# Performance work log

Hardware: AMD Instinct MI355X
Metric: run time of the kernel (lower is better)

The kernel has to match this reference:

```python
import jax, jax.numpy as jnp
import numpy as np

N_NODES = 100000
N_EDGES = 1600000
D = 128
N_LAYERS = 3  # GIN num_layers = n_layers + 1 with n_layers = 2
BN_EPS = 1e-5


def _batchnorm(x, gamma, beta):
    # Training-mode BatchNorm1d over the node axis (biased variance, as torch uses
    # for normalization).
    mean = jnp.mean(x, axis=0)
    var = jnp.mean((x - mean) ** 2, axis=0)
    return (x - mean) * jax.lax.rsqrt(var + BN_EPS) * gamma + beta


def setup_inputs() -> dict:
    key = jax.random.key(0)
    ks = jax.random.split(key, 5)
    features = jax.random.normal(ks[0], (N_NODES, D), dtype=jnp.float32)
    W = jax.random.normal(ks[1], (N_LAYERS, D, D), dtype=jnp.float32) * 0.05
    b = jnp.zeros((N_LAYERS, D), dtype=jnp.float32)
    eps = jnp.zeros((N_LAYERS,), dtype=jnp.float32)  # learn_eps init 0
    bn1_gamma = jnp.ones((N_LAYERS, D), dtype=jnp.float32)
    bn1_beta = jnp.zeros((N_LAYERS, D), dtype=jnp.float32)
    bn2_gamma = jnp.ones((N_LAYERS, D), dtype=jnp.float32)
    bn2_beta = jnp.zeros((N_LAYERS, D), dtype=jnp.float32)
    src = jax.random.randint(ks[2], (N_EDGES,), 0, N_NODES, dtype=jnp.int64 if jax.config.jax_enable_x64 else jnp.int32)
    dst = jax.random.randint(ks[3], (N_EDGES,), 0, N_NODES, dtype=jnp.int64 if jax.config.jax_enable_x64 else jnp.int32)
    return {
        'features': features, 'W': W, 'b': b, 'eps': eps,
        'bn1_gamma': bn1_gamma, 'bn1_beta': bn1_beta,
        'bn2_gamma': bn2_gamma, 'bn2_beta': bn2_beta,
        'src': src, 'dst': dst,
    }


def reference(features, W, b, eps, bn1_gamma, bn1_beta, bn2_gamma, bn2_beta, src, dst):
    n = features.shape[0]
    h = features
    hidden_rep = [h]
    for i in range(N_LAYERS):
        # GINConv, 'sum' aggregation: (1+eps)*h_v + sum_{u->v} h_u
        agg = jax.ops.segment_sum(h[src], dst, num_segments=n)
        z = (1.0 + eps[i]) * h + agg
        # ApplyNodeFunc: Linear (num_mlp_layers=1) -> BN -> ReLU
        z = z @ W[i] + b[i]
        z = jax.nn.relu(_batchnorm(z, bn1_gamma[i], bn1_beta[i]))
        # GIN.forward: outer BN -> ReLU
        z = jax.nn.relu(_batchnorm(z, bn2_gamma[i], bn2_beta[i]))
        h = z
        hidden_rep.append(h)
    # torch.stack(hidden_rep) -> [n_layers+2, N, D]
    return jnp.stack(hidden_rep, axis=0)
```

## Files before the change

### kernel.cpp

```cpp
#include <hip/hip_runtime.h>
#include <hip/hip_bf16.h>

#define DD 128

typedef __attribute__((ext_vector_type(8))) short bfrag8;
typedef __attribute__((ext_vector_type(4))) float f32x4;

__device__ __forceinline__ float bf16lo(unsigned int u) {
    union { unsigned int i; float f; } c; c.i = u << 16; return c.f;
}
__device__ __forceinline__ float bf16hi(unsigned int u) {
    union { unsigned int i; float f; } c; c.i = u & 0xffff0000u; return c.f;
}
__device__ __forceinline__ float bf16f(unsigned short u) {
    union { unsigned int i; float f; } c; c.i = ((unsigned int)u) << 16; return c.f;
}
__device__ __forceinline__ unsigned short f2bf(float f) {
    union { float f; unsigned int i; } c; c.f = f;
    unsigned int x = c.i;
    unsigned int r = (x + 0x7fffu + ((x >> 16) & 1u)) >> 16;
    return (unsigned short)r;
}

__global__ void k_setup(const int* __restrict__ dst, int* __restrict__ deg, int E,
                        const float* __restrict__ features, float* __restrict__ out0,
                        unsigned int* __restrict__ hb, int total4,
                        const float* __restrict__ W, unsigned short* __restrict__ Wt) {
    int gtid = blockIdx.x * blockDim.x + threadIdx.x;
    int gsz = gridDim.x * blockDim.x;
    for (int i = gtid; i < E; i += gsz) atomicAdd(&deg[dst[i]], 1);
    for (int i = gtid; i < total4; i += gsz) {
        float4 v = ((const float4*)features)[i];
        ((float4*)out0)[i] = v;
        unsigned int lo = (unsigned int)f2bf(v.x) | ((unsigned int)f2bf(v.y) << 16);
        unsigned int hi = (unsigned int)f2bf(v.z) | ((unsigned int)f2bf(v.w) << 16);
        ((uint2*)hb)[i] = make_uint2(lo, hi);
    }
    for (int i = gtid; i < 3 * 128 * 128; i += gsz) {
        int l = i >> 14, r = i & 16383, k = r >> 7, n = r & 127;
        Wt[(l << 14) + n * 128 + k] = f2bf(W[i]);
    }
}

__global__ void k_scan1(const int* __restrict__ deg, int* __restrict__ partials, int Nn) {
    __shared__ int sm[256];
    int tid = threadIdx.x;
    int base = (blockIdx.x << 10) + 4 * tid;
    int s = 0;
    if (base + 3 < Nn) {
        int4 v = *(const int4*)&deg[base];
        s = v.x + v.y + v.z + v.w;
    } else {
        for (int j = 0; j < 4; j++) if (base + j < Nn) s += deg[base + j];
    }
    sm[tid] = s;
    __syncthreads();
    for (int off = 128; off > 0; off >>= 1) {
        if (tid < off) sm[tid] += sm[tid + off];
        __syncthreads();
    }
    if (tid == 0) partials[blockIdx.x] = sm[0];
}

__global__ void k_scan3(const int* __restrict__ deg, const int* __restrict__ partials,
                        int* __restrict__ row_start, int Nn, int E, int nchunk) {
    __shared__ int sp[256];
    __shared__ int sm[256];
    int tid = threadIdx.x, c = blockIdx.x;
    int p = (tid < nchunk) ? partials[tid] : 0;
    sp[tid] = p;
    __syncthreads();
    for (int off = 1; off < 256; off <<= 1) {
        int t = (tid >= off) ? sp[tid - off] : 0;
        __syncthreads();
        sp[tid] += t;
        __syncthreads();
    }
    int chunkpref = (c == 0) ? 0 : sp[c - 1];

    int base = (c << 10) + 4 * tid;
    int d0 = 0, d1 = 0, d2 = 0, d3 = 0;
    if (base + 3 < Nn) {
        int4 v = *(const int4*)&deg[base];
        d0 = v.x; d1 = v.y; d2 = v.z; d3 = v.w;
    } else {
        if (base + 0 < Nn) d0 = deg[base + 0];
        if (base + 1 < Nn) d1 = deg[base + 1];
        if (base + 2 < Nn) d2 = deg[base + 2];
        if (base + 3 < Nn) d3 = deg[base + 3];
    }
    int ts = d0 + d1 + d2 + d3;
    sm[tid] = ts;
    __syncthreads();
    for (int off = 1; off < 256; off <<= 1) {
        int t = (tid >= off) ? sm[tid - off] : 0;
        __syncthreads();
        sm[tid] += t;
        __syncthreads();
    }
    int run = chunkpref + sm[tid] - ts;
    if (base + 0 < Nn) row_start[base + 0] = run; run += d0;
    if (base + 1 < Nn) row_start[base + 1] = run; run += d1;
    if (base + 2 < Nn) row_start[base + 2] = run; run += d2;
    if (base + 3 < Nn) row_start[base + 3] = run;
    if (c == 0 && tid == 0) row_start[Nn] = E;
}

__global__ void k_scatter(const int* __restrict__ src, const int* __restrict__ dst,
                          const int* __restrict__ row_start, int* __restrict__ cursor,
                          int* __restrict__ csr, int E) {
    int i = blockIdx.x * blockDim.x + threadIdx.x;
    if (i < E) {
        int d = dst[i];
        int pos = row_start[d] + atomicAdd(&cursor[d], 1);
        csr[pos] = src[i];
    }
}

__device__ __forceinline__ void acc_u4(float* acc, uint4 a) {
    acc[0] += bf16lo(a.x); acc[1] += bf16hi(a.x);
    acc[2] += bf16lo(a.y); acc[3] += bf16hi(a.y);
    acc[4] += bf16lo(a.z); acc[5] += bf16hi(a.z);
    acc[6] += bf16lo(a.w); acc[7] += bf16hi(a.w);
}

__global__ void k_gather(const unsigned int* __restrict__ hb, const int* __restrict__ row_start,
                         const int* __restrict__ csr, const float* __restrict__ eps, int layer,
                         unsigned int* __restrict__ zb, int Nn) {
    int wv = threadIdx.x >> 6, lane = threadIdx.x & 63;
    int v = blockIdx.x * 4 + wv;
    if (v >= Nn) return;
    int q = lane & 15;
    int slot = lane >> 4;
    const uint4* hb4 = (const uint4*)hb;
    float acc[8];
    #pragma unroll
    for (int j = 0; j < 8; j++) acc[j] = 0.f;

    int beg = row_start[v], end = row_start[v + 1];
    int e = beg;
    for (; e + 15 < end; e += 16) {
        int u0 = csr[e + slot];
        int u1 = csr[e + 4 + slot];
        int u2 = csr[e + 8 + slot];
        int u3 = csr[e + 12 + slot];
        uint4 a = hb4[(size_t)u0 * 16 + q];
        uint4 b = hb4[(size_t)u1 * 16 + q];
        uint4 c = hb4[(size_t)u2 * 16 + q];
        uint4 d = hb4[(size_t)u3 * 16 + q];
        acc_u4(acc, a); acc_u4(acc, b); acc_u4(acc, c); acc_u4(acc, d);
    }
    for (; e + 3 < end; e += 4) {
        int u = csr[e + slot];
        uint4 a = hb4[(size_t)u * 16 + q];
        acc_u4(acc, a);
    }
    {
        int r = end - e;
        if (slot < r) {
            int u = csr[e + slot];
            uint4 a = hb4[(size_t)u * 16 + q];
            acc_u4(acc, a);
        }
    }
    #pragma unroll
    for (int j = 0; j < 8; j++) {
        acc[j] += __shfl_xor(acc[j], 16);
        acc[j] += __shfl_xor(acc[j], 32);
    }
    if (slot == 0) {
        float e1 = 1.0f + eps[layer];
        uint4 hs = hb4[(size_t)v * 16 + q];
        float f0 = acc[0] + e1 * bf16lo(hs.x);
        float f1 = acc[1] + e1 * bf16hi(hs.x);
        float f2 = acc[2] + e1 * bf16lo(hs.y);
        float f3 = acc[3] + e1 * bf16hi(hs.y);
        float f4 = acc[4] + e1 * bf16lo(hs.z);
        float f5 = acc[5] + e1 * bf16hi(hs.z);
        float f6 = acc[6] + e1 * bf16lo(hs.w);
        float f7 = acc[7] + e1 * bf16hi(hs.w);
        uint4 o;
        o.x = (unsigned int)f2bf(f0) | ((unsigned int)f2bf(f1) << 16);
        o.y = (unsigned int)f2bf(f2) | ((unsigned int)f2bf(f3) << 16);
        o.z = (unsigned int)f2bf(f4) | ((unsigned int)f2bf(f5) << 16);
        o.w = (unsigned int)f2bf(f6) | ((unsigned int)f2bf(f7) << 16);
        ((uint4*)zb)[(size_t)v * 16 + q] = o;
    }
}

__launch_bounds__(256)
__global__ void k_gemm(const unsigned short* __restrict__ zb, const unsigned short* __restrict__ Wt,
                       const float* __restrict__ bias, int layer, unsigned short* __restrict__ yb,
                       float* __restrict__ stl, int Nn) {
    __shared__ unsigned short Al[64 * 136];
    int tid = threadIdx.x;
    int m0 = blockIdx.x * 64;
    #pragma unroll
    for (int p = 0; p < 4; p++) {
        int slot = p * 256 + tid;
        int r = slot >> 4, c = slot & 15;
        int grow = m0 + r;
        uint4 val = make_uint4(0, 0, 0, 0);
        if (grow < Nn) val = *(const uint4*)&zb[(size_t)grow * 128 + c * 8];
        *(uint4*)&Al[r * 136 + c * 8] = val;
    }
    __syncthreads();

    int lane = tid & 63, wv = tid >> 6;
    int tcol = lane & 15, quad = lane >> 4;
    const unsigned short* Wl = Wt + (layer << 14);
    f32x4 acc[4][2];
    #pragma unroll
    for (int a = 0; a < 4; a++)
        #pragma unroll
        for (int b2 = 0; b2 < 2; b2++) acc[a][b2] = (f32x4){0.f, 0.f, 0.f, 0.f};

    #pragma unroll
    for (int kk = 0; kk < 128; kk += 32) {
        int kb = kk + quad * 8;
        bfrag8 af[4], bf[2];
        #pragma unroll
        for (int mt = 0; mt < 4; mt++)
            af[mt] = *(const bfrag8*)&Al[(16 * mt + tcol) * 136 + kb];
        #pragma unroll
        for (int nt = 0; nt < 2; nt++)
            bf[nt] = *(const bfrag8*)&Wl[(32 * wv + 16 * nt + tcol) * 128 + kb];
        #pragma unroll
        for (int mt = 0; mt < 4; mt++)
            #pragma unroll
            for (int nt = 0; nt < 2; nt++)
                acc[mt][nt] = __builtin_amdgcn_mfma_f32_16x16x32_bf16(af[mt], bf[nt], acc[mt][nt], 0, 0, 0);
    }

    #pragma unroll
    for (int nt = 0; nt < 2; nt++) {
        int col = 32 * wv + 16 * nt + tcol;
        float bcol = bias[layer * 128 + col];
        float psum = 0.f, psq = 0.f;
        #pragma unroll
        for (int mt = 0; mt < 4; mt++) {
            #pragma unroll
            for (int r = 0; r < 4; r++) {
                int row = m0 + 16 * mt + quad * 4 + r;
                if (row < Nn) {
                    unsigned short u = f2bf(acc[mt][nt][r] + bcol);
                    yb[(size_t)row * 128 + col] = u;
                    float vr = bf16f(u);
                    psum += vr;
                    psq += vr * vr;
                }
            }
        }
        psum += __shfl_xor(psum, 16); psq += __shfl_xor(psq, 16);
        psum += __shfl_xor(psum, 32); psq += __shfl_xor(psq, 32);
        if (lane < 16) {
            atomicAdd(&stl[col], psum);
            atomicAdd(&stl[128 + col], psq);
        }
    }
}

__launch_bounds__(256)
__global__ void k_stats2(const unsigned short* __restrict__ yb, float* __restrict__ stl,
                         const float* __restrict__ g1, const float* __restrict__ b1,
                         int layer, int totalU8, float invN) {
    __shared__ float red[512];
    int tid = threadIdx.x;
    if (tid < 128) {
        float m = stl[tid] * invN;
        float var = stl[128 + tid] * invN - m * m;
        float rstd = rsqrtf(var + 1e-5f);
        float s = g1[layer * 128 + tid] * rstd;
        red[tid] = s;
        red[128 + tid] = b1[layer * 128 + tid] - m * s;
        red[256 + tid] = 0.f;
        red[384 + tid] = 0.f;
    }
    __syncthreads();
    int lane = tid & 63;
    int cbase = (8 * tid) & 127;
    float s1r[8], sh1r[8];
    #pragma unroll
    for (int j = 0; j < 8; j++) { s1r[j] = red[cbase + j]; sh1r[j] = red[128 + cbase + j]; }
    float ps[8], pq[8];
    #pragma unroll
    for (int j = 0; j < 8; j++) { ps[j] = 0.f; pq[j] = 0.f; }
    int gtid = blockIdx.x * 256 + tid;
    int gsz = gridDim.x * 256;
    const uint4* yb4 = (const uint4*)yb;
    for (int i = gtid; i < totalU8; i += gsz) {
        uint4 v = yb4[i];
        float f[8];
        f[0] = bf16lo(v.x); f[1] = bf16hi(v.x);
        f[2] = bf16lo(v.y); f[3] = bf16hi(v.y);
        f[4] = bf16lo(v.z); f[5] = bf16hi(v.z);
        f[6] = bf16lo(v.w); f[7] = bf16hi(v.w);
        #pragma unroll
        for (int j = 0; j < 8; j++) {
            float t = fmaxf(f[j] * s1r[j] + sh1r[j], 0.f);
            ps[j] += t; pq[j] += t * t;
        }
    }
    #pragma unroll
    for (int j = 0; j < 8; j++) {
        ps[j] += __shfl_xor(ps[j], 16);
        pq[j] += __shfl_xor(pq[j], 16);
        ps[j] += __shfl_xor(ps[j], 32);
        pq[j] += __shfl_xor(pq[j], 32);
    }
    if (lane < 16) {
        #pragma unroll
        for (int j = 0; j < 8; j++) {
            atomicAdd(&red[256 + cbase + j], ps[j]);
            atomicAdd(&red[384 + cbase + j], pq[j]);
        }
    }
    __syncthreads();
    if (tid < 128) {
        atomicAdd(&stl[256 + tid], red[256 + tid]);
        atomicAdd(&stl[384 + tid], red[384 + tid]);
    }
}

__launch_bounds__(256)
__global__ void k_apply(const unsigned short* __restrict__ yb, const float* __restrict__ stl,
                        const float* __restrict__ g1, const float* __restrict__ b1,
                        const float* __restrict__ g2, const float* __restrict__ b2,
                        int layer, float* __restrict__ outl, unsigned int* __restrict__ hb,
                        int totalU8, float invN) {
    __shared__ float red[512];
    int tid = threadIdx.x;
    if (tid < 128) {
        float m1 = stl[tid] * invN;
        float v1 = stl[128 + tid] * invN - m1 * m1;
        float r1 = rsqrtf(v1 + 1e-5f);
        float s1 = g1[layer * 128 + tid] * r1;
        red[tid] = s1;
        red[128 + tid] = b1[layer * 128 + tid] - m1 * s1;
        float m2 = stl[256 + tid] * invN;
        float v2 = stl[384 + tid] * invN - m2 * m2;
        float r2 = rsqrtf(v2 + 1e-5f);
        float s2 = g2[layer * 128 + tid] * r2;
        red[256 + tid] = s2;
        red[384 + tid] = b2[layer * 128 + tid] - m2 * s2;
    }
    __syncthreads();
    int cbase = (8 * tid) & 127;
    float s1a[8], sh1a[8], s2a[8], sh2a[8];
    #pragma unroll
    for (int j = 0; j < 8; j++) {
        s1a[j]  = red[cbase + j];       sh1a[j] = red[128 + cbase + j];
        s2a[j]  = red[256 + cbase + j]; sh2a[j] = red[384 + cbase + j];
    }
    int gtid = blockIdx.x * 256 + tid;
    int gsz = gridDim.x * 256;
    const uint4* yb4 = (const uint4*)yb;
    for (int i = gtid; i < totalU8; i += gsz) {
        uint4 v = yb4[i];
        float f[8];
        f[0] = bf16lo(v.x); f[1] = bf16hi(v.x);
        f[2] = bf16lo(v.y); f[3] = bf16hi(v.y);
        f[4] = bf16lo(v.z); f[5] = bf16hi(v.z);
        f[6] = bf16lo(v.w); f[7] = bf16hi(v.w);
        float o[8];
        #pragma unroll
        for (int j = 0; j < 8; j++) {
            float t = fmaxf(f[j] * s1a[j] + sh1a[j], 0.f);
            o[j] = fmaxf(t * s2a[j] + sh2a[j], 0.f);
        }
        ((float4*)outl)[2 * i]     = make_float4(o[0], o[1], o[2], o[3]);
        ((float4*)outl)[2 * i + 1] = make_float4(o[4], o[5], o[6], o[7]);
        uint4 hbv;
        hbv.x = (unsigned int)f2bf(o[0]) | ((unsigned int)f2bf(o[1]) << 16);
        hbv.y = (unsigned int)f2bf(o[2]) | ((unsigned int)f2bf(o[3]) << 16);
        hbv.z = (unsigned int)f2bf(o[4]) | ((unsigned int)f2bf(o[5]) << 16);
        hbv.w = (unsigned int)f2bf(o[6]) | ((unsigned int)f2bf(o[7]) << 16);
        ((uint4*)hb)[i] = hbv;
    }
}

extern "C" void kernel_launch(void* const* d_in, const int* in_sizes, int n_in,
                              void* d_out, int out_size, void* d_ws, size_t ws_size,
                              hipStream_t stream) {
    const float* features = (const float*)d_in[0];
    const float* W        = (const float*)d_in[1];
    const float* bias     = (const float*)d_in[2];
    const float* eps      = (const float*)d_in[3];
    const float* g1       = (const float*)d_in[4];
    const float* b1       = (const float*)d_in[5];
    const float* g2       = (const float*)d_in[6];
    const float* b2       = (const float*)d_in[7];
    const int*   src      = (const int*)d_in[8];
    const int*   dst      = (const int*)d_in[9];

    const int Nn = in_sizes[0] / DD;
    const int E  = in_sizes[8];
    float* out = (float*)d_out;

    char* w = (char*)d_ws;
    auto alloc = [&](size_t bytes) -> char* {
        char* p = w;
        w += (bytes + 255) & ~(size_t)255;
        return p;
    };
    int*   deg    = (int*)alloc((size_t)Nn * 4);
    int*   cursor = (int*)alloc((size_t)Nn * 4);
    float* stats  = (float*)alloc(3 * 512 * 4);
    char*  zero_end = w;
    int* row_start = (int*)alloc((size_t)(Nn + 1) * 4);
    int* partials  = (int*)alloc(1024);
    int* csr       = (int*)alloc((size_t)E * 4);
    unsigned int* hb = (unsigned int*)alloc((size_t)Nn * 64 * 4);
    unsigned int* zb = (unsigned int*)alloc((size_t)Nn * 64 * 4);
    unsigned short* Wt = (unsigned short*)alloc((size_t)3 * 128 * 128 * 2);
    unsigned short* yb = (unsigned short*)alloc((size_t)Nn * 128 * 2);

    const int total4 = Nn * DD / 4;
    const int totalU8 = Nn * DD / 8;
    const float invN = 1.0f / (float)Nn;
    const int nchunk = (Nn + 1023) / 1024;

    hipMemsetAsync(deg, 0, (size_t)(zero_end - (char*)deg), stream);

    k_setup<<<(E + 255) / 256, 256, 0, stream>>>(dst, deg, E, features, out, hb, total4, W, Wt);
    k_scan1<<<nchunk, 256, 0, stream>>>(deg, partials, Nn);
    k_scan3<<<nchunk, 256, 0, stream>>>(deg, partials, row_start, Nn, E, nchunk);
    k_scatter<<<(E + 255) / 256, 256, 0, stream>>>(src, dst, row_start, cursor, csr, E);

    for (int l = 0; l < 3; l++) {
        float* stl = stats + l * 512;
        float* outl = out + (size_t)(l + 1) * Nn * DD;
        k_gather<<<(Nn + 3) / 4, 256, 0, stream>>>(hb, row_start, csr, eps, l, zb, Nn);
        k_gemm<<<(Nn + 63) / 64, 256, 0, stream>>>((const unsigned short*)zb, Wt, bias, l, yb,
                                                   stl, Nn);
        k_stats2<<<512, 256, 0, stream>>>(yb, stl, g1, b1, l, totalU8, invN);
        k_apply<<<1024, 256, 0, stream>>>(yb, stl, g1, b1, g2, b2, l, outl, hb, totalU8, invN);
    }
}
```

Baseline: 833.8 us.

## Fuse GEMM, BN stats and apply into one persistent kernel with grid barriers

Replaces the separate GEMM, second-BN-stats and apply kernels with one kernel per layer. Each block computes two 64-row tiles, keeps the bf16 results in registers, and uses two software grid barriers to wait for the global BN statistics before applying the normalisations. This removes the yb round trip through global memory and two launches. The risks are a deadlock if all ~782 blocks cannot be co-resident (launch bounds 256,4 over 256 CUs), and that the final stores are now scalar and less coalesced.

```diff
diff --git a/kernel.cpp b/kernel.cpp
--- a/kernel.cpp
+++ b/kernel.cpp
@@ -188,13 +188,13 @@
     }
 }
 
-__launch_bounds__(256)
-__global__ void k_gemm(const unsigned short* __restrict__ zb, const unsigned short* __restrict__ Wt,
-                       const float* __restrict__ bias, int layer, unsigned short* __restrict__ yb,
-                       float* __restrict__ stl, int Nn) {
-    __shared__ unsigned short Al[64 * 136];
-    int tid = threadIdx.x;
-    int m0 = blockIdx.x * 64;
+__device__ __forceinline__ void layer_tile(const unsigned short* __restrict__ zb,
+                                           const unsigned short* __restrict__ Wl,
+                                           const float* __restrict__ bias, int layer,
+                                           float* __restrict__ stl, unsigned short* Al,
+                                           int m0, int Nn, int tid, int lane, int wv,
+                                           int tcol, int quad, unsigned int (&ypk)[4][2][2]) {
+    __syncthreads();
     #pragma unroll
     for (int p = 0; p < 4; p++) {
         int slot = p * 256 + tid;
@@ -206,9 +206,6 @@
     }
     __syncthreads();
 
-    int lane = tid & 63, wv = tid >> 6;
-    int tcol = lane & 15, quad = lane >> 4;
-    const unsigned short* Wl = Wt + (layer << 14);
     f32x4 acc[4][2];
     #pragma unroll
     for (int a = 0; a < 4; a++)
@@ -239,17 +236,18 @@
         float psum = 0.f, psq = 0.f;
         #pragma unroll
         for (int mt = 0; mt < 4; mt++) {
-            #pragma unroll
-            for (int r = 0; r < 4; r++) {
-                int row = m0 + 16 * mt + quad * 4 + r;
-                if (row < Nn) {
-                    unsigned short u = f2bf(acc[mt][nt][r] + bcol);
-                    yb[(size_t)row * 128 + col] = u;
-                    float vr = bf16f(u);
-                    psum += vr;
-                    psq += vr * vr;
-                }
-            }
+            unsigned short u0 = f2bf(acc[mt][nt][0] + bcol);
+            unsigned short u1 = f2bf(acc[mt][nt][1] + bcol);
+            unsigned short u2 = f2bf(acc[mt][nt][2] + bcol);
+            unsigned short u3 = f2bf(acc[mt][nt][3] + bcol);
+            ypk[mt][nt][0] = (unsigned int)u0 | ((unsigned int)u1 << 16);
+            ypk[mt][nt][1] = (unsigned int)u2 | ((unsigned int)u3 << 16);
+            int rowb = m0 + 16 * mt + quad * 4;
+            float v0 = bf16f(u0), v1 = bf16f(u1), v2 = bf16f(u2), v3 = bf16f(u3);
+            if (rowb + 0 < Nn) { psum += v0; psq += v0 * v0; }
+            if (rowb + 1 < Nn) { psum += v1; psq += v1 * v1; }
+            if (rowb + 2 < Nn) { psum += v2; psq += v2 * v2; }
+            if (rowb + 3 < Nn) { psum += v3; psq += v3 * v3; }
         }
         psum += __shfl_xor(psum, 16); psq += __shfl_xor(psq, 16);
         psum += __shfl_xor(psum, 32); psq += __shfl_xor(psq, 32);
@@ -260,122 +258,174 @@
     }
 }
 
-__launch_bounds__(256)
-__global__ void k_stats2(const unsigned short* __restrict__ yb, float* __restrict__ stl,
-                         const float* __restrict__ g1, const float* __restrict__ b1,
-                         int layer, int totalU8, float invN) {
-    __shared__ float red[512];
-    int tid = threadIdx.x;
-    if (tid < 128) {
-        float m = stl[tid] * invN;
-        float var = stl[128 + tid] * invN - m * m;
-        float rstd = rsqrtf(var + 1e-5f);
-        float s = g1[layer * 128 + tid] * rstd;
-        red[tid] = s;
-        red[128 + tid] = b1[layer * 128 + tid] - m * s;
-        red[256 + tid] = 0.f;
-        red[384 + tid] = 0.f;
-    }
-    __syncthreads();
-    int lane = tid & 63;
-    int cbase = (8 * tid) & 127;
-    float s1r[8], sh1r[8];
-    #pragma unroll
-    for (int j = 0; j < 8; j++) { s1r[j] = red[cbase + j]; sh1r[j] = red[128 + cbase + j]; }
-    float ps[8], pq[8];
-    #pragma unroll
-    for (int j = 0; j < 8; j++) { ps[j] = 0.f; pq[j] = 0.f; }
-    int gtid = blockIdx.x * 256 + tid;
-    int gsz = gridDim.x * 256;
-    const uint4* yb4 = (const uint4*)yb;
-    for (int i = gtid; i < totalU8; i += gsz) {
-        uint4 v = yb4[i];
-        float f[8];
-        f[0] = bf16lo(v.x); f[1] = bf16hi(v.x);
-        f[2] = bf16lo(v.y); f[3] = bf16hi(v.y);
-        f[4] = bf16lo(v.z); f[5] = bf16hi(v.z);
-        f[6] = bf16lo(v.w); f[7] = bf16hi(v.w);
-        #pragma unroll
-        for (int j = 0; j < 8; j++) {
-            float t = fmaxf(f[j] * s1r[j] + sh1r[j], 0.f);
-            ps[j] += t; pq[j] += t * t;
-        }
-    }
-    #pragma unroll
-    for (int j = 0; j < 8; j++) {
-        ps[j] += __shfl_xor(ps[j], 16);
-        pq[j] += __shfl_xor(pq[j], 16);
-        ps[j] += __shfl_xor(ps[j], 32);
-        pq[j] += __shfl_xor(pq[j], 32);
-    }
-    if (lane < 16) {
-        #pragma unroll
-        for (int j = 0; j < 8; j++) {
-            atomicAdd(&red[256 + cbase + j], ps[j]);
-            atomicAdd(&red[384 + cbase + j], pq[j]);
-        }
-    }
-    __syncthreads();
-    if (tid < 128) {
-        atomicAdd(&stl[256 + tid], red[256 + tid]);
-        atomicAdd(&stl[384 + tid], red[384 + tid]);
-    }
-}
-
-__launch_bounds__(256)
-__global__ void k_apply(const unsigned short* __restrict__ yb, const float* __restrict__ stl,
+__device__ __forceinline__ void grid_barrier(int* ctr, int nb, int tid) {
+    __syncthreads();
+    if (tid == 0) {
+        __threadfence();
+        atomicAdd(ctr, 1);
+        while (__hip_atomic_load(ctr, __ATOMIC_ACQUIRE, __HIP_MEMORY_SCOPE_AGENT) < nb)
+            __builtin_amdgcn_s_sleep(2);
+    }
+    __syncthreads();
+}
+
+__launch_bounds__(256, 4)
+__global__ void k_layer(const unsigned short* __restrict__ zb,
+                        const unsigned short* __restrict__ Wt,
+                        const float* __restrict__ bias,
                         const float* __restrict__ g1, const float* __restrict__ b1,
                         const float* __restrict__ g2, const float* __restrict__ b2,
-                        int layer, float* __restrict__ outl, unsigned int* __restrict__ hb,
-                        int totalU8, float invN) {
-    __shared__ float red[512];
-    int tid = threadIdx.x;
+                        int layer, float* __restrict__ stl,
+                        int* __restrict__ ctr1, int* __restrict__ ctr2, int nb,
+                        float* __restrict__ outl, unsigned short* __restrict__ hb16,
+                        int Nn, int ntiles, float invN) {
+    __shared__ unsigned short Al[64 * 136];
+    __shared__ float param[512];
+    __shared__ float red[256];
+    int tid = threadIdx.x, lane = tid & 63, wv = tid >> 6;
+    int tcol = lane & 15, quad = lane >> 4;
+    const unsigned short* Wl = Wt + (layer << 14);
+    int t0 = 2 * (int)blockIdx.x;
+    int m0A = t0 * 64, m0B = m0A + 64;
+    bool hasB = (t0 + 1) < ntiles;
+
+    unsigned int yA[4][2][2], yB[4][2][2];
+    #pragma unroll
+    for (int mt = 0; mt < 4; mt++)
+        #pragma unroll
+        for (int nt = 0; nt < 2; nt++) { yB[mt][nt][0] = 0; yB[mt][nt][1] = 0; }
+
+    layer_tile(zb, Wl, bias, layer, stl, Al, m0A, Nn, tid, lane, wv, tcol, quad, yA);
+    if (hasB)
+        layer_tile(zb, Wl, bias, layer, stl, Al, m0B, Nn, tid, lane, wv, tcol, quad, yB);
+
+    grid_barrier(ctr1, nb, tid);
+
     if (tid < 128) {
-        float m1 = stl[tid] * invN;
-        float v1 = stl[128 + tid] * invN - m1 * m1;
-        float r1 = rsqrtf(v1 + 1e-5f);
-        float s1 = g1[layer * 128 + tid] * r1;
-        red[tid] = s1;
-        red[128 + tid] = b1[layer * 128 + tid] - m1 * s1;
-        float m2 = stl[256 + tid] * invN;
-        float v2 = stl[384 + tid] * invN - m2 * m2;
-        float r2 = rsqrtf(v2 + 1e-5f);
-        float s2 = g2[layer * 128 + tid] * r2;
-        red[256 + tid] = s2;
-        red[384 + tid] = b2[layer * 128 + tid] - m2 * s2;
-    }
-    __syncthreads();
-    int cbase = (8 * tid) & 127;
-    float s1a[8], sh1a[8], s2a[8], sh2a[8];
-    #pragma unroll
-    for (int j = 0; j < 8; j++) {
-        s1a[j]  = red[cbase + j];       sh1a[j] = red[128 + cbase + j];
-        s2a[j]  = red[256 + cbase + j]; sh2a[j] = red[384 + cbase + j];
-    }
-    int gtid = blockIdx.x * 256 + tid;
-    int gsz = gridDim.x * 256;
-    const uint4* yb4 = (const uint4*)yb;
-    for (int i = gtid; i < totalU8; i += gsz) {
-        uint4 v = yb4[i];
-        float f[8];
-        f[0] = bf16lo(v.x); f[1] = bf16hi(v.x);
-        f[2] = bf16lo(v.y); f[3] = bf16hi(v.y);
-        f[4] = bf16lo(v.z); f[5] = bf16hi(v.z);
-        f[6] = bf16lo(v.w); f[7] = bf16hi(v.w);
-        float o[8];
-        #pragma unroll
-        for (int j = 0; j < 8; j++) {
-            float t = fmaxf(f[j] * s1a[j] + sh1a[j], 0.f);
-            o[j] = fmaxf(t * s2a[j] + sh2a[j], 0.f);
-        }
-        ((float4*)outl)[2 * i]     = make_float4(o[0], o[1], o[2], o[3]);
-        ((float4*)outl)[2 * i + 1] = make_float4(o[4], o[5], o[6], o[7]);
-        uint4 hbv;
-        hbv.x = (unsigned int)f2bf(o[0]) | ((unsigned int)f2bf(o[1]) << 16);
-        hbv.y = (unsigned int)f2bf(o[2]) | ((unsigned int)f2bf(o[3]) << 16);
-        hbv.z = (unsigned int)f2bf(o[4]) | ((unsigned int)f2bf(o[5]) << 16);
-        hbv.w = (unsigned int)f2bf(o[6]) | ((unsigned int)f2bf(o[7]) << 16);
-        ((uint4*)hb)[i] = hbv;
+        float s  = __hip_atomic_load(&stl[tid], __ATOMIC_RELAXED, __HIP_MEMORY_SCOPE_AGENT);
+        float sq = __hip_atomic_load(&stl[128 + tid], __ATOMIC_RELAXED, __HIP_MEMORY_SCOPE_AGENT);
+        float m = s * invN, var = sq * invN - m * m;
+        float rs = rsqrtf(var + 1e-5f);
+        float sc = g1[layer * 128 + tid] * rs;
+        param[tid] = sc;
+        param[128 + tid] = b1[layer * 128 + tid] - m * sc;
+    }
+    red[tid] = 0.f;
+    __syncthreads();
+
+    float s1[2], sh1[2];
+    #pragma unroll
+    for (int nt = 0; nt < 2; nt++) {
+        int col = 32 * wv + 16 * nt + tcol;
+        s1[nt] = param[col];
+        sh1[nt] = param[128 + col];
+    }
+    float ps[2] = {0.f, 0.f}, pq[2] = {0.f, 0.f};
+    #pragma unroll
+    for (int nt = 0; nt < 2; nt++) {
+        #pragma unroll
+        for (int mt = 0; mt < 4; mt++) {
+            int rowbA = m0A + 16 * mt + quad * 4;
+            float v0 = bf16lo(yA[mt][nt][0]), v1 = bf16hi(yA[mt][nt][0]);
+            float v2 = bf16lo(yA[mt][nt][1]), v3 = bf16hi(yA[mt][nt][1]);
+            if (rowbA + 0 < Nn) { float t = fmaxf(v0 * s1[nt] + sh1[nt], 0.f); ps[nt] += t; pq[nt] += t * t; }
+            if (rowbA + 1 < Nn) { float t = fmaxf(v1 * s1[nt] + sh1[nt], 0.f); ps[nt] += t; pq[nt] += t * t; }
+            if (rowbA + 2 < Nn) { float t = fmaxf(v2 * s1[nt] + sh1[nt], 0.f); ps[nt] += t; pq[nt] += t * t; }
+            if (rowbA + 3 < Nn) { float t = fmaxf(v3 * s1[nt] + sh1[nt], 0.f); ps[nt] += t; pq[nt] += t * t; }
+        }
+    }
+    if (hasB) {
+        #pragma unroll
+        for (int nt = 0; nt < 2; nt++) {
+            #pragma unroll
+            for (int mt = 0; mt < 4; mt++) {
+                int rowbB = m0B + 16 * mt + quad * 4;
+                float v0 = bf16lo(yB[mt][nt][0]), v1 = bf16hi(yB[mt][nt][0]);
+                float v2 = bf16lo(yB[mt][nt][1]), v3 = bf16hi(yB[mt][nt][1]);
+                if (rowbB + 0 < Nn) { float t = fmaxf(v0 * s1[nt] + sh1[nt], 0.f); ps[nt] += t; pq[nt] += t * t; }
+                if (rowbB + 1 < Nn) { float t = fmaxf(v1 * s1[nt] + sh1[nt], 0.f); ps[nt] += t; pq[nt] += t * t; }
+                if (rowbB + 2 < Nn) { float t = fmaxf(v2 * s1[nt] + sh1[nt], 0.f); ps[nt] += t; pq[nt] += t * t; }
+                if (rowbB + 3 < Nn) { float t = fmaxf(v3 * s1[nt] + sh1[nt], 0.f); ps[nt] += t; pq[nt] += t * t; }
+            }
+        }
+    }
+    #pragma unroll
+    for (int nt = 0; nt < 2; nt++) {
+        float a = ps[nt], b = pq[nt];
+        a += __shfl_xor(a, 16); b += __shfl_xor(b, 16);
+        a += __shfl_xor(a, 32); b += __shfl_xor(b, 32);
+        if (lane < 16) {
+            int col = 32 * wv + 16 * nt + tcol;
+            atomicAdd(&red[col], a);
+            atomicAdd(&red[128 + col], b);
+        }
+    }
+    __syncthreads();
+    if (tid < 128) {
+        atomicAdd(&stl[256 + tid], red[tid]);
+        atomicAdd(&stl[384 + tid], red[128 + tid]);
+    }
+
+    grid_barrier(ctr2, nb, tid);
+
+    if (tid < 128) {
+        float s  = __hip_atomic_load(&stl[256 + tid], __ATOMIC_RELAXED, __HIP_MEMORY_SCOPE_AGENT);
+        float sq = __hip_atomic_load(&stl[384 + tid], __ATOMIC_RELAXED, __HIP_MEMORY_SCOPE_AGENT);
+        float m = s * invN, var = sq * invN - m * m;
+        float rs = rsqrtf(var + 1e-5f);
+        float sc = g2[layer * 128 + tid] * rs;
+        param[256 + tid] = sc;
+        param[384 + tid] = b2[layer * 128 + tid] - m * sc;
+    }
+    __syncthreads();
+    float s2[2], sh2[2];
+    #pragma unroll
+    for (int nt = 0; nt < 2; nt++) {
+        int col = 32 * wv + 16 * nt + tcol;
+        s2[nt] = param[256 + col];
+        sh2[nt] = param[384 + col];
+    }
+    #pragma unroll
+    for (int nt = 0; nt < 2; nt++) {
+        int col = 32 * wv + 16 * nt + tcol;
+        #pragma unroll
+        for (int mt = 0; mt < 4; mt++) {
+            int rowb = m0A + 16 * mt + quad * 4;
+            float v[4] = { bf16lo(yA[mt][nt][0]), bf16hi(yA[mt][nt][0]),
+                           bf16lo(yA[mt][nt][1]), bf16hi(yA[mt][nt][1]) };
+            #pragma unroll
+            for (int r = 0; r < 4; r++) {
+                int row = rowb + r;
+                if (row < Nn) {
+                    float t = fmaxf(v[r] * s1[nt] + sh1[nt], 0.f);
+                    float o = fmaxf(t * s2[nt] + sh2[nt], 0.f);
+                    outl[(size_t)row * 128 + col] = o;
+                    hb16[(size_t)row * 128 + col] = f2bf(o);
+                }
+            }
+        }
+    }
+    if (hasB) {
+        #pragma unroll
+        for (int nt = 0; nt < 2; nt++) {
+            int col = 32 * wv + 16 * nt + tcol;
+            #pragma unroll
+            for (int mt = 0; mt < 4; mt++) {
+                int rowb = m0B + 16 * mt + quad * 4;
+                float v[4] = { bf16lo(yB[mt][nt][0]), bf16hi(yB[mt][nt][0]),
+                               bf16lo(yB[mt][nt][1]), bf16hi(yB[mt][nt][1]) };
+                #pragma unroll
+                for (int r = 0; r < 4; r++) {
+                    int row = rowb + r;
+                    if (row < Nn) {
+                        float t = fmaxf(v[r] * s1[nt] + sh1[nt], 0.f);
+                        float o = fmaxf(t * s2[nt] + sh2[nt], 0.f);
+                        outl[(size_t)row * 128 + col] = o;
+                        hb16[(size_t)row * 128 + col] = f2bf(o);
+                    }
+                }
+            }
+        }
     }
 }
 
@@ -406,6 +456,7 @@
     int*   deg    = (int*)alloc((size_t)Nn * 4);
     int*   cursor = (int*)alloc((size_t)Nn * 4);
     float* stats  = (float*)alloc(3 * 512 * 4);
+    int*   syncs  = (int*)alloc(8 * 4);
     char*  zero_end = w;
     int* row_start = (int*)alloc((size_t)(Nn + 1) * 4);
     int* partials  = (int*)alloc(1024);
@@ -413,12 +464,12 @@
     unsigned int* hb = (unsigned int*)alloc((size_t)Nn * 64 * 4);
     unsigned int* zb = (unsigned int*)alloc((size_t)Nn * 64 * 4);
     unsigned short* Wt = (unsigned short*)alloc((size_t)3 * 128 * 128 * 2);
-    unsigned short* yb = (unsigned short*)alloc((size_t)Nn * 128 * 2);
 
     const int total4 = Nn * DD / 4;
-    const int totalU8 = Nn * DD / 8;
     const float invN = 1.0f / (float)Nn;
     const int nchunk = (Nn + 1023) / 1024;
+    const int ntiles = (Nn + 63) / 64;
+    const int nlb = (ntiles + 1) / 2;
 
     hipMemsetAsync(deg, 0, (size_t)(zero_end - (char*)deg), stream);
 
@@ -431,9 +482,8 @@
         float* stl = stats + l * 512;
         float* outl = out + (size_t)(l + 1) * Nn * DD;
         k_gather<<<(Nn + 3) / 4, 256, 0, stream>>>(hb, row_start, csr, eps, l, zb, Nn);
-        k_gemm<<<(Nn + 63) / 64, 256, 0, stream>>>((const unsigned short*)zb, Wt, bias, l, yb,
-                                                   stl, Nn);
-        k_stats2<<<512, 256, 0, stream>>>(yb, stl, g1, b1, l, totalU8, invN);
-        k_apply<<<1024, 256, 0, stream>>>(yb, stl, g1, b1, g2, b2, l, outl, hb, totalU8, invN);
-    }
-}
+        k_layer<<<nlb, 256, 0, stream>>>((const unsigned short*)zb, Wt, bias, g1, b1, g2, b2,
+                                         l, stl, syncs + 2 * l, syncs + 2 * l + 1, nlb,
+                                         outl, (unsigned short*)hb, Nn, ntiles, invN);
+    }
+}
```

Result: slower. 1.165 ms (+39.8%).
